# Kernel optimization log

Hardware: AMD Instinct MI355X
Metric: run time of the kernel (lower is better)

## Reference

```python
import jax, jax.numpy as jnp
import numpy as np

B, C, H, W = 4, 64, 64, 64
CQ = C // 2

def setup_inputs() -> dict:
    key = jax.random.key(0)
    ks = jax.random.split(key, 7)
    return {
        "x":  jax.random.normal(ks[0], (B, C, H, W), dtype=jnp.float32),
        "Wq": jax.random.normal(ks[1], (CQ, C), dtype=jnp.float32) * 0.05,
        "bq": jax.random.normal(ks[2], (CQ,), dtype=jnp.float32) * 0.05,
        "Wk": jax.random.normal(ks[3], (CQ, C), dtype=jnp.float32) * 0.05,
        "bk": jax.random.normal(ks[4], (CQ,), dtype=jnp.float32) * 0.05,
        "Wl": jax.random.normal(ks[5], (C, C), dtype=jnp.float32) * 0.05,
        "bl": jax.random.normal(ks[6], (C,), dtype=jnp.float32) * 0.05,
    }

def reference(x, Wq, bq, Wk, bk, Wl, bl):
    b, c, h, w = x.shape
    hw = h * w
    xf = x.reshape(b, c, hw)                                   # [B,C,HW]
    # 1x1 convs == per-pixel linear projections
    q = jnp.einsum('oc,bci->boi', Wq, xf) + bq[None, :, None]  # [B,CQ,HW]
    k = jnp.einsum('oc,bci->boi', Wk, xf) + bk[None, :, None]  # [B,CQ,HW]
    # energy[b,i,j] = <q[:,i], k[:,j]>  (proj_query permuted to [B,HW,CQ])
    energy = jnp.einsum('bci,bcj->bij', q, k)                  # [B,HW,HW]
    attn = jax.nn.softmax(energy, axis=-1)                     # softmax over last dim (keys j)
    # torch.bmm(proj_value, attention): out[b,c,j] = sum_i value[b,c,i] * attn[b,i,j]
    out = jnp.einsum('bci,bij->bcj', xf, attn)                 # [B,C,HW]
    out = out.reshape(b, c, h, w)
    out = jnp.einsum('oc,bchw->bohw', Wl, out) + bl[None, :, None, None]
    return out + x
```

## Files before the change

kernel.cpp:

```cpp
#include <hip/hip_runtime.h>
#include <hip/hip_bf16.h>


#define HW 4096
#define BN 4
#define CD 64
#define ISPL 8
#define LOG2E 1.44269504f

typedef short bf16x8 __attribute__((ext_vector_type(8)));
typedef float f32x4 __attribute__((ext_vector_type(4)));

static __device__ inline unsigned bfbits(float f) {
    union { float f; unsigned u; } v{f};
    return (v.u + 0x8000u) >> 16;
}
static __device__ inline float b2f(short s) {
    unsigned u = ((unsigned)(unsigned short)s) << 16;
    float f; __builtin_memcpy(&f, &u, 4); return f;
}
static __device__ inline int cvtpk(float lo, float hi) {
    __hip_bfloat162 h = __float22bfloat162_rn(make_float2(lo, hi));
    int r; __builtin_memcpy(&r, &h, 4); return r;
}
static __device__ inline void gl16(const void* g, void* l) {
    __builtin_amdgcn_global_load_lds(
        (const __attribute__((address_space(1))) unsigned int*)g,
        (__attribute__((address_space(3))) unsigned int*)l, 16, 0, 0);
}



__global__ __launch_bounds__(256, 4) void k_proj(
    const float* __restrict__ x, const float* __restrict__ Wq, const float* __restrict__ bq,
    const float* __restrict__ Wk, const float* __restrict__ bk, const float* __restrict__ Wl,
    short* __restrict__ Qt, short* __restrict__ Kt, short* __restrict__ Yc)
{
    __shared__ __align__(16) char sm[18944];
    short* WcL   = (short*)sm;
    short* xT    = (short*)(sm + 16384);
    float* biasL = (float*)(sm + 18432);

    int t = threadIdx.x;
    int wv = t >> 6, l = t & 63, g = l >> 4, n = l & 15;

    {
        int row = t >> 1, half = t & 1;
        const float* src; float scale = 1.f;
        if (row < 32)      { src = Wq + row * CD; scale = LOG2E; }
        else if (row < 64) { src = Wk + (row - 32) * CD; }
        else               { src = Wl + (row - 64) * CD; }
        int pk[16];
#pragma unroll
        for (int e = 0; e < 16; ++e)
            pk[e] = cvtpk(src[half * 32 + 2 * e] * scale, src[half * 32 + 2 * e + 1] * scale);
#pragma unroll
        for (int q = 0; q < 4; ++q)
            *(int4*)(WcL + row * 64 + ((((half << 2) + q) ^ (row & 7)) << 3)) =
                make_int4(pk[4 * q], pk[4 * q + 1], pk[4 * q + 2], pk[4 * q + 3]);
        if (half == 0)
            biasL[row] = (row < 32) ? LOG2E * bq[row] : (row < 64) ? bk[row - 32] : 0.f;
    }
    int pix0 = blockIdx.x << 4;
    {
        int c = t >> 2, q = t & 3;
        int b = pix0 >> 12, pxb = pix0 & (HW - 1);
        float4 v = *(const float4*)(x + ((size_t)b << 18) + ((size_t)c << 12) + pxb + q * 4);
        float vv[4] = {v.x, v.y, v.z, v.w};
#pragma unroll
        for (int e = 0; e < 4; ++e) {
            int px = q * 4 + e;
            xT[px * 64 + (((c >> 3) ^ (px & 7)) << 3) + (c & 7)] = (short)bfbits(vv[e]);
        }
    }
    __syncthreads();

    bf16x8 B0 = *(const bf16x8*)(xT + n * 64 + ((g ^ (n & 7)) << 3));
    bf16x8 B1 = *(const bf16x8*)(xT + n * 64 + (((4 + g) ^ (n & 7)) << 3));
    int pg = pix0 + n;
#pragma unroll
    for (int mm = 0; mm < 2; ++mm) {
        int mt = wv * 2 + mm;
        bf16x8 A0 = *(const bf16x8*)(WcL + (mt * 16 + n) * 64 + ((g ^ (n & 7)) << 3));
        bf16x8 A1 = *(const bf16x8*)(WcL + (mt * 16 + n) * 64 + (((4 + g) ^ (n & 7)) << 3));
        f32x4 d = {0.f, 0.f, 0.f, 0.f};
        d = __builtin_amdgcn_mfma_f32_16x16x32_bf16(A0, B0, d, 0, 0, 0);
        d = __builtin_amdgcn_mfma_f32_16x16x32_bf16(A1, B1, d, 0, 0, 0);
        d += *(const f32x4*)(biasL + mt * 16 + g * 4);
        if (mt < 4) {
            short* dst = (mt < 2 ? Qt : Kt) + ((size_t)pg << 5) + ((mt & 1) << 4) + (g << 2);
            *(int2*)dst = make_int2(cvtpk(d[0], d[1]), cvtpk(d[2], d[3]));
        } else {
            int ch2 = (mt - 4) * 16 + g * 4;
            int bb = pg >> 12, ii = pg & (HW - 1);
#pragma unroll
            for (int r = 0; r < 4; ++r)
                Yc[(((size_t)(bb * CD + ch2 + r)) << 12) + ii] = (short)bfbits(d[r]);
        }
    }
}


__global__ __launch_bounds__(256, 4) void k_pass1m(
    const short* __restrict__ Qt, const short* __restrict__ Kt, float* __restrict__ mrow)
{
    __shared__ __align__(16) char sm1[33792];
    short* KL  = (short*)sm1;
    float* red = (float*)(sm1 + 32768);

    int t = threadIdx.x;
    int wv = t >> 6, l = t & 63, g = l >> 4, n = l & 15;
    int ch = blockIdx.x;
    int b = ch & 3, i0 = (ch >> 2) << 6;
    size_t bHW = (size_t)b << 12;

    bf16x8 aq[4];
#pragma unroll
    for (int it = 0; it < 4; ++it)
        aq[it] = *(const bf16x8*)(Qt + ((bHW + i0 + it * 16 + n) << 5) + (g << 3));

    const char* ksrc = (const char*)(Kt + (bHW << 5));

    f32x4 ls[4];
#pragma unroll
    for (int it = 0; it < 4; ++it) ls[it] = (f32x4){0.f, 0.f, 0.f, 0.f};

#pragma unroll
    for (int q = 0; q < 4; ++q) {
        int off = (wv * 4 + q) * 1024 + l * 16;
        gl16(ksrc + off, (char*)KL + off);
    }
    asm volatile("s_waitcnt vmcnt(0)" ::: "memory");
    __builtin_amdgcn_s_barrier();
    __builtin_amdgcn_sched_barrier(0);

    const int NCH = 16;
    for (int chk = 0; chk < NCH; ++chk) {
        int cur = chk & 1;
        if (chk > 0) {
            __builtin_amdgcn_s_barrier();
            __builtin_amdgcn_sched_barrier(0);
        }
        if (chk + 1 < NCH) {
#pragma unroll
            for (int q = 0; q < 4; ++q) {
                int off = (wv * 4 + q) * 1024 + l * 16;
                gl16(ksrc + (size_t)(chk + 1) * 16384 + off,
                     (char*)KL + (cur ^ 1) * 16384 + off);
            }
            asm volatile("s_waitcnt vmcnt(4)" ::: "memory");
        } else {
            asm volatile("s_waitcnt vmcnt(0)" ::: "memory");
        }
        __builtin_amdgcn_sched_barrier(0);

        const short* kb = (const short*)((char*)KL + cur * 16384);
#pragma unroll
        for (int jj = 0; jj < 4; ++jj) {
            bf16x8 bkv = *(const bf16x8*)(kb + (((wv * 4 + jj) * 16 + n) << 5) + (g << 3));
#pragma unroll
            for (int it = 0; it < 4; ++it) {
                f32x4 z = {0.f, 0.f, 0.f, 0.f};
                f32x4 s = __builtin_amdgcn_mfma_f32_16x16x32_bf16(aq[it], bkv, z, 0, 0, 0);
                ls[it][0] += exp2f(s[0]); ls[it][1] += exp2f(s[1]);
                ls[it][2] += exp2f(s[2]); ls[it][3] += exp2f(s[3]);
            }
        }
        __builtin_amdgcn_sched_barrier(0);
    }

#pragma unroll
    for (int msk = 1; msk < 16; msk <<= 1)
#pragma unroll
        for (int it = 0; it < 4; ++it) {
            ls[it][0] += __shfl_xor(ls[it][0], msk, 64);
            ls[it][1] += __shfl_xor(ls[it][1], msk, 64);
            ls[it][2] += __shfl_xor(ls[it][2], msk, 64);
            ls[it][3] += __shfl_xor(ls[it][3], msk, 64);
        }
    if (n == 0)
#pragma unroll
        for (int it = 0; it < 4; ++it)
#pragma unroll
            for (int r = 0; r < 4; ++r)
                red[wv * 64 + it * 16 + g * 4 + r] = ls[it][r];
    __syncthreads();
    if (t < 64) {
        float s = red[t] + red[64 + t] + red[128 + t] + red[192 + t];
        mrow[bHW + i0 + t] = -log2f(s);
    }
}


__global__ __launch_bounds__(256, 4) void k_pass2(
    const short* __restrict__ Qt, const short* __restrict__ Kt,
    const short* __restrict__ Yc, const float* __restrict__ mrow,
    short* __restrict__ Opart)
{
    __shared__ __align__(16) char smem[36864];
    short* QtL = (short*)smem;
    short* W2L = (short*)(smem + 8192);
    short* Pb  = (short*)(smem + 24576);
    float* MtA = (float*)(smem + 34816);

    int t = threadIdx.x;
    int wv = t >> 6, l = t & 63, g = l >> 4, n = l & 15;
    int ch = blockIdx.x;
    int b = ch >> 8, isp = (ch >> 5) & 7, jt = ch & 31;
    int j0 = jt * 128 + wv * 32;
    size_t bHW = (size_t)b << 12;
    short* Pw = Pb + wv * 1280;

    bf16x8 bk0 = *(const bf16x8*)(Kt + ((bHW + j0 + n) << 5) + (g << 3));
    bf16x8 bk1 = *(const bf16x8*)(Kt + ((bHW + j0 + 16 + n) << 5) + (g << 3));

    f32x4 oacc[2][4];
#pragma unroll
    for (int a = 0; a < 2; ++a)
#pragma unroll
        for (int m = 0; m < 4; ++m) oacc[a][m] = (f32x4){0.f, 0.f, 0.f, 0.f};

    int swz = ((t & 7) ^ ((t >> 3) & 7)) << 4;
    const char* qsrc = (const char*)Qt + ((bHW + (size_t)isp * 512) << 6) + t * 16;
    const char* wsrc = (const char*)Yc + (((size_t)(b * CD + (t >> 3)) << 12) + isp * 512) * 2 + swz;
    char* qd0 = (char*)QtL + t * 16;  char* qd1 = qd0 + 4096;
    char* wd0 = (char*)W2L + t * 16;  char* wd1 = wd0 + 8192;

    gl16(qsrc, qd0);
    gl16(wsrc, wd0);
    gl16(wsrc + (32ull << 13), wd0 + 4096);
    if (t < 128)
        gl16((const char*)(mrow + bHW + (size_t)isp * 512) + t * 16, (char*)MtA + t * 16);
    asm volatile("s_waitcnt vmcnt(0)" ::: "memory");
    __builtin_amdgcn_s_barrier();
    __builtin_amdgcn_sched_barrier(0);

    const int NT = 8;
    for (int st = 0; st < NT; ++st) {
        int cur = st & 1;
        if (st > 0) {
            __builtin_amdgcn_s_barrier();
            __builtin_amdgcn_sched_barrier(0);
        }
        if (st + 1 < NT) {
            gl16(qsrc + (size_t)(st + 1) * 4096, cur ? qd0 : qd1);
            gl16(wsrc + (size_t)(st + 1) * 128, cur ? wd0 : wd1);
            gl16(wsrc + (size_t)(st + 1) * 128 + (32ull << 13), (cur ? wd0 : wd1) + 4096);
            asm volatile("s_waitcnt vmcnt(3)" ::: "memory");
        } else {
            asm volatile("s_waitcnt vmcnt(0)" ::: "memory");
        }
        __builtin_amdgcn_sched_barrier(0);

        const short* qL = QtL + cur * 2048;
        const char* wL = (const char*)W2L + cur * 8192;
        const float* mL = MtA + st * 64;
#pragma unroll
        for (int ks = 0; ks < 2; ++ks) {
            bf16x8 aq0 = *(const bf16x8*)(qL + (ks * 32 + n) * 32 + g * 8);
            bf16x8 aq1 = *(const bf16x8*)(qL + (ks * 32 + 16 + n) * 32 + g * 8);
            f32x4 cm0 = *(const f32x4*)(mL + ks * 32 + g * 4);
            f32x4 cm1 = *(const f32x4*)(mL + ks * 32 + 16 + g * 4);
            __builtin_amdgcn_s_setprio(1);
            f32x4 s00 = __builtin_amdgcn_mfma_f32_16x16x32_bf16(aq0, bk0, cm0, 0, 0, 0);
            f32x4 s01 = __builtin_amdgcn_mfma_f32_16x16x32_bf16(aq1, bk0, cm1, 0, 0, 0);
            f32x4 s10 = __builtin_amdgcn_mfma_f32_16x16x32_bf16(aq0, bk1, cm0, 0, 0, 0);
            f32x4 s11 = __builtin_amdgcn_mfma_f32_16x16x32_bf16(aq1, bk1, cm1, 0, 0, 0);
            __builtin_amdgcn_s_setprio(0);
            *(int2*)(Pw + n * 40 + 4 * g) =
                make_int2(cvtpk(exp2f(s00[0]), exp2f(s00[1])), cvtpk(exp2f(s00[2]), exp2f(s00[3])));
            *(int2*)(Pw + n * 40 + 16 + 4 * g) =
                make_int2(cvtpk(exp2f(s01[0]), exp2f(s01[1])), cvtpk(exp2f(s01[2]), exp2f(s01[3])));
            *(int2*)(Pw + (16 + n) * 40 + 4 * g) =
                make_int2(cvtpk(exp2f(s10[0]), exp2f(s10[1])), cvtpk(exp2f(s10[2]), exp2f(s10[3])));
            *(int2*)(Pw + (16 + n) * 40 + 16 + 4 * g) =
                make_int2(cvtpk(exp2f(s11[0]), exp2f(s11[1])), cvtpk(exp2f(s11[2]), exp2f(s11[3])));
            bf16x8 pb0 = *(const bf16x8*)(Pw + n * 40 + 8 * g);
            bf16x8 pb1 = *(const bf16x8*)(Pw + (16 + n) * 40 + 8 * g);
            __builtin_amdgcn_s_setprio(1);
#pragma unroll
            for (int mb = 0; mb < 4; ++mb) {
                bf16x8 aw = *(const bf16x8*)(wL + (mb * 16 + n) * 128 + ((((ks << 2) + g) ^ (n & 7)) << 4));
                oacc[0][mb] = __builtin_amdgcn_mfma_f32_16x16x32_bf16(aw, pb0, oacc[0][mb], 0, 0, 0);
                oacc[1][mb] = __builtin_amdgcn_mfma_f32_16x16x32_bf16(aw, pb1, oacc[1][mb], 0, 0, 0);
            }
            __builtin_amdgcn_s_setprio(0);
        }
        __builtin_amdgcn_sched_barrier(0);
    }
    size_t obase = ((((size_t)isp * BN + b) * CD) << 12) + j0 + n;
#pragma unroll
    for (int j2 = 0; j2 < 2; ++j2)
#pragma unroll
        for (int mb = 0; mb < 4; ++mb)
#pragma unroll
            for (int r = 0; r < 4; ++r)
                Opart[obase + (((size_t)(mb * 16 + g * 4 + r)) << 12) + j2 * 16] =
                    (short)bfbits(oacc[j2][mb][r]);
}


__global__ __launch_bounds__(256, 4) void k_merge(
    const short* __restrict__ Opart, const float* __restrict__ x,
    const float* __restrict__ bl, float* __restrict__ out)
{
    int t = threadIdx.x;
    int e = (blockIdx.x * 256 + t) * 4;
    int c = (e >> 12) & 63;
    float4 r = *(const float4*)(x + e);
    float bc = bl[c];
    r.x += bc; r.y += bc; r.z += bc; r.w += bc;
#pragma unroll
    for (int p = 0; p < ISPL; ++p) {
        int2 o4 = *(const int2*)(Opart + ((size_t)p << 20) + e);
        r.x += b2f((short)(o4.x & 0xffff));
        r.y += b2f((short)(o4.x >> 16));
        r.z += b2f((short)(o4.y & 0xffff));
        r.w += b2f((short)(o4.y >> 16));
    }
    *(float4*)(out + e) = r;
}

extern "C" void kernel_launch(void* const* d_in, const int* in_sizes, int n_in,
                              void* d_out, int out_size, void* d_ws, size_t ws_size,
                              hipStream_t stream)
{
    (void)in_sizes; (void)n_in; (void)out_size; (void)ws_size;
    const float* x  = (const float*)d_in[0];
    const float* Wq = (const float*)d_in[1];
    const float* bq = (const float*)d_in[2];
    const float* Wk = (const float*)d_in[3];
    const float* bk = (const float*)d_in[4];
    const float* Wl = (const float*)d_in[5];
    const float* bl = (const float*)d_in[6];
    float* out = (float*)d_out;
    char* base = (char*)d_ws;

    short* Qt    = (short*)(base);
    short* Kt    = (short*)(base + 0x100000);
    short* Yc    = (short*)(base + 0x200000);
    float* mrow  = (float*)(base + 0x500000);
    short* Opart = (short*)(base + 0x510000);

    hipLaunchKernelGGL(k_proj, dim3(1024), dim3(256), 0, stream,
                       x, Wq, bq, Wk, bk, Wl, Qt, Kt, Yc);
    hipLaunchKernelGGL(k_pass1m, dim3(256), dim3(256), 0, stream, Qt, Kt, mrow);
    hipLaunchKernelGGL(k_pass2, dim3(1024), dim3(256), 0, stream,
                       Qt, Kt, Yc, mrow, Opart);
    hipLaunchKernelGGL(k_merge, dim3(1024), dim3(256), 0, stream, Opart, x, bl, out);
}
```

Baseline: 69.33 us.

## Split softmax row-sum pass over key quarters and drop LDS staging

```diff
diff --git a/kernel.cpp b/kernel.cpp
--- a/kernel.cpp
+++ b/kernel.cpp
@@ -102,16 +102,13 @@
 
 
 __global__ __launch_bounds__(256, 4) void k_pass1m(
-    const short* __restrict__ Qt, const short* __restrict__ Kt, float* __restrict__ mrow)
-{
-    __shared__ __align__(16) char sm1[33792];
-    short* KL  = (short*)sm1;
-    float* red = (float*)(sm1 + 32768);
-
+    const short* __restrict__ Qt, const short* __restrict__ Kt, float* __restrict__ Spart)
+{
+    __shared__ float red[256];
     int t = threadIdx.x;
     int wv = t >> 6, l = t & 63, g = l >> 4, n = l & 15;
     int ch = blockIdx.x;
-    int b = ch & 3, i0 = (ch >> 2) << 6;
+    int b = ch & 3, jq = (ch >> 2) & 3, i0 = (ch >> 4) << 6;
     size_t bHW = (size_t)b << 12;
 
     bf16x8 aq[4];
@@ -119,56 +116,22 @@
     for (int it = 0; it < 4; ++it)
         aq[it] = *(const bf16x8*)(Qt + ((bHW + i0 + it * 16 + n) << 5) + (g << 3));
 
-    const char* ksrc = (const char*)(Kt + (bHW << 5));
-
     f32x4 ls[4];
 #pragma unroll
     for (int it = 0; it < 4; ++it) ls[it] = (f32x4){0.f, 0.f, 0.f, 0.f};
 
-#pragma unroll
-    for (int q = 0; q < 4; ++q) {
-        int off = (wv * 4 + q) * 1024 + l * 16;
-        gl16(ksrc + off, (char*)KL + off);
-    }
-    asm volatile("s_waitcnt vmcnt(0)" ::: "memory");
-    __builtin_amdgcn_s_barrier();
-    __builtin_amdgcn_sched_barrier(0);
-
-    const int NCH = 16;
-    for (int chk = 0; chk < NCH; ++chk) {
-        int cur = chk & 1;
-        if (chk > 0) {
-            __builtin_amdgcn_s_barrier();
-            __builtin_amdgcn_sched_barrier(0);
-        }
-        if (chk + 1 < NCH) {
-#pragma unroll
-            for (int q = 0; q < 4; ++q) {
-                int off = (wv * 4 + q) * 1024 + l * 16;
-                gl16(ksrc + (size_t)(chk + 1) * 16384 + off,
-                     (char*)KL + (cur ^ 1) * 16384 + off);
-            }
-            asm volatile("s_waitcnt vmcnt(4)" ::: "memory");
-        } else {
-            asm volatile("s_waitcnt vmcnt(0)" ::: "memory");
-        }
-        __builtin_amdgcn_sched_barrier(0);
-
-        const short* kb = (const short*)((char*)KL + cur * 16384);
-#pragma unroll
-        for (int jj = 0; jj < 4; ++jj) {
-            bf16x8 bkv = *(const bf16x8*)(kb + (((wv * 4 + jj) * 16 + n) << 5) + (g << 3));
-#pragma unroll
-            for (int it = 0; it < 4; ++it) {
-                f32x4 z = {0.f, 0.f, 0.f, 0.f};
-                f32x4 s = __builtin_amdgcn_mfma_f32_16x16x32_bf16(aq[it], bkv, z, 0, 0, 0);
-                ls[it][0] += exp2f(s[0]); ls[it][1] += exp2f(s[1]);
-                ls[it][2] += exp2f(s[2]); ls[it][3] += exp2f(s[3]);
-            }
-        }
-        __builtin_amdgcn_sched_barrier(0);
-    }
-
+    const short* kbase = Kt + ((bHW + jq * 1024 + wv * 256 + n) << 5) + (g << 3);
+#pragma unroll 4
+    for (int jt = 0; jt < 16; ++jt) {
+        bf16x8 bkv = *(const bf16x8*)(kbase + jt * 512);
+#pragma unroll
+        for (int it = 0; it < 4; ++it) {
+            f32x4 z = {0.f, 0.f, 0.f, 0.f};
+            f32x4 s = __builtin_amdgcn_mfma_f32_16x16x32_bf16(aq[it], bkv, z, 0, 0, 0);
+            ls[it][0] += exp2f(s[0]); ls[it][1] += exp2f(s[1]);
+            ls[it][2] += exp2f(s[2]); ls[it][3] += exp2f(s[3]);
+        }
+    }
 #pragma unroll
     for (int msk = 1; msk < 16; msk <<= 1)
 #pragma unroll
@@ -187,14 +150,14 @@
     __syncthreads();
     if (t < 64) {
         float s = red[t] + red[64 + t] + red[128 + t] + red[192 + t];
-        mrow[bHW + i0 + t] = -log2f(s);
+        Spart[(size_t)jq * 16384 + bHW + i0 + t] = s;
     }
 }
 
 
 __global__ __launch_bounds__(256, 4) void k_pass2(
     const short* __restrict__ Qt, const short* __restrict__ Kt,
-    const short* __restrict__ Yc, const float* __restrict__ mrow,
+    const short* __restrict__ Yc, const float* __restrict__ Spart,
     short* __restrict__ Opart)
 {
     __shared__ __align__(16) char smem[36864];
@@ -229,9 +192,20 @@
     gl16(qsrc, qd0);
     gl16(wsrc, wd0);
     gl16(wsrc + (32ull << 13), wd0 + 4096);
-    if (t < 128)
-        gl16((const char*)(mrow + bHW + (size_t)isp * 512) + t * 16, (char*)MtA + t * 16);
-    asm volatile("s_waitcnt vmcnt(0)" ::: "memory");
+    if (t < 128) {
+        const float* sp = Spart + bHW + (size_t)isp * 512 + t * 4;
+        float4 a0 = *(const float4*)(sp);
+        float4 a1 = *(const float4*)(sp + 16384);
+        float4 a2 = *(const float4*)(sp + 32768);
+        float4 a3 = *(const float4*)(sp + 49152);
+        float4 mm;
+        mm.x = -log2f(a0.x + a1.x + a2.x + a3.x);
+        mm.y = -log2f(a0.y + a1.y + a2.y + a3.y);
+        mm.z = -log2f(a0.z + a1.z + a2.z + a3.z);
+        mm.w = -log2f(a0.w + a1.w + a2.w + a3.w);
+        *(float4*)(MtA + t * 4) = mm;
+    }
+    asm volatile("s_waitcnt vmcnt(0) lgkmcnt(0)" ::: "memory");
     __builtin_amdgcn_s_barrier();
     __builtin_amdgcn_sched_barrier(0);
 
@@ -339,13 +313,13 @@
     short* Qt    = (short*)(base);
     short* Kt    = (short*)(base + 0x100000);
     short* Yc    = (short*)(base + 0x200000);
-    float* mrow  = (float*)(base + 0x500000);
-    short* Opart = (short*)(base + 0x510000);
+    float* Spart = (float*)(base + 0x500000);
+    short* Opart = (short*)(base + 0x540000);
 
     hipLaunchKernelGGL(k_proj, dim3(1024), dim3(256), 0, stream,
                        x, Wq, bq, Wk, bk, Wl, Qt, Kt, Yc);
-    hipLaunchKernelGGL(k_pass1m, dim3(256), dim3(256), 0, stream, Qt, Kt, mrow);
+    hipLaunchKernelGGL(k_pass1m, dim3(1024), dim3(256), 0, stream, Qt, Kt, Spart);
     hipLaunchKernelGGL(k_pass2, dim3(1024), dim3(256), 0, stream,
-                       Qt, Kt, Yc, mrow, Opart);
+                       Qt, Kt, Yc, Spart, Opart);
     hipLaunchKernelGGL(k_merge, dim3(1024), dim3(256), 0, stream, Opart, x, bl, out);
 }
```

Result: faster. 62.31 us (-10.1%).
